# Kernel tuning notes

Measured on AMD Instinct MI355X. Metric: run time of the kernel, lower is better.

Reference implementation:

```python
import jax, jax.numpy as jnp
import numpy as np

B, S, D = 16, 2048, 64
SCALE = 1.0 / np.sqrt(np.float32(D))  # forward divides by sqrt(embedding_dim=64)


def setup_inputs() -> dict:
    key = jax.random.key(0)
    ks = jax.random.split(key, 7)
    return {
        "x": jax.random.normal(ks[0], (B, S, D), dtype=jnp.float32),
        "Wq": jax.random.normal(ks[1], (D, D), dtype=jnp.float32) * 0.02,
        "bq": jax.random.normal(ks[2], (D,), dtype=jnp.float32) * 0.02,
        "Wk": jax.random.normal(ks[3], (D, D), dtype=jnp.float32) * 0.02,
        "bk": jax.random.normal(ks[4], (D,), dtype=jnp.float32) * 0.02,
        "Wv": jax.random.normal(ks[5], (D, D), dtype=jnp.float32) * 0.02,
        "bv": jax.random.normal(ks[6], (D,), dtype=jnp.float32) * 0.02,
    }


def reference(x, Wq, bq, Wk, bk, Wv, bv):
    # Linear projections (weights stored [in, out], math-equivalent to nn.Linear)
    q = jnp.einsum("bsd,de->bse", x, Wq) + bq
    k = jnp.einsum("bsd,de->bse", x, Wk) + bk
    v = jnp.einsum("bsd,de->bse", x, Wv) + bv
    # Unfused scores: [B, S, S]
    scores = jnp.einsum("bqd,bkd->bqk", q, k) * jnp.float32(SCALE)
    causal = jnp.tril(jnp.ones((S, S), dtype=bool))  # mask[:S,:S]
    scores = jnp.where(causal, scores, jnp.float32(-jnp.inf))
    attn = jax.nn.softmax(scores, axis=-1)
    # dropout is identity in eval mode (reference baseline)
    out = jnp.einsum("bqk,bkd->bqd", attn, v)
    return out
```

## Files before the change

kernel.cpp:

```cpp
#include <hip/hip_runtime.h>

#define NB 16
#define SS 2048
#define DD 64

typedef __attribute__((ext_vector_type(8))) short short8;
typedef __attribute__((ext_vector_type(4))) float f32x4;

#define SCL2E 0.18033688011112042f

__device__ __forceinline__ short f2bf(float f) {
  union { float f; unsigned u; } v; v.f = f;
  unsigned r = (v.u + 0x7fffu + ((v.u >> 16) & 1u)) >> 16;
  return (short)r;
}

__device__ __forceinline__ short8 load_a_frag_f32(const float* p) {
  float4 u = *(const float4*)p;
  float4 w = *(const float4*)(p + 4);
  short8 r;
  r[0] = f2bf(u.x); r[1] = f2bf(u.y); r[2] = f2bf(u.z); r[3] = f2bf(u.w);
  r[4] = f2bf(w.x); r[5] = f2bf(w.y); r[6] = f2bf(w.z); r[7] = f2bf(w.w);
  return r;
}

__global__ __launch_bounds__(256) void proj_kernel(
    const float* __restrict__ x,
    const float* __restrict__ Wq, const float* __restrict__ bq,
    const float* __restrict__ Wk, const float* __restrict__ bk,
    const float* __restrict__ Wv, const float* __restrict__ bv,
    ushort* __restrict__ qo, ushort* __restrict__ ko, ushort* __restrict__ vT)
{
  __shared__ __align__(16) ushort Wt[3][64][72];
  __shared__ __align__(16) ushort Vs[64][68];
  const int t = threadIdx.x;
  {
    const float* Ws[3] = {Wq, Wk, Wv};
    for (int m = 0; m < 3; ++m)
      for (int i = 0; i < 4; ++i) {
        int idx = i * 1024 + t * 4;
        int kk = idx >> 6, n0 = idx & 63;
        float4 w4 = *(const float4*)(Ws[m] + kk * 64 + n0);
        Wt[m][n0 + 0][kk] = (ushort)f2bf(w4.x);
        Wt[m][n0 + 1][kk] = (ushort)f2bf(w4.y);
        Wt[m][n0 + 2][kk] = (ushort)f2bf(w4.z);
        Wt[m][n0 + 3][kk] = (ushort)f2bf(w4.w);
      }
  }
  __syncthreads();

  const int lane = t & 63, w = t >> 6;
  const int l15 = lane & 15, quad = lane >> 4;
  const int g = blockIdx.x * 64 + w * 16 + l15;
  short8 a0 = load_a_frag_f32(x + (size_t)g * 64 + quad * 8);
  short8 a1 = load_a_frag_f32(x + (size_t)g * 64 + 32 + quad * 8);
  const int lrow0 = w * 16 + quad * 4;
  const int row0 = blockIdx.x * 64 + lrow0;

  for (int m = 0; m < 3; ++m) {
    const float* bp = (m == 0 ? bq : (m == 1 ? bk : bv));
    for (int nt = 0; nt < 4; ++nt) {
      short8 b0 = *(const short8*)&Wt[m][nt * 16 + l15][quad * 8];
      short8 b1 = *(const short8*)&Wt[m][nt * 16 + l15][32 + quad * 8];
      f32x4 acc = {0.f, 0.f, 0.f, 0.f};
      acc = __builtin_amdgcn_mfma_f32_16x16x32_bf16(a0, b0, acc, 0, 0, 0);
      acc = __builtin_amdgcn_mfma_f32_16x16x32_bf16(a1, b1, acc, 0, 0, 0);
      float bb = bp[nt * 16 + l15];
      if (m == 0) {
        for (int r = 0; r < 4; ++r)
          qo[(size_t)(row0 + r) * 64 + nt * 16 + l15] = (ushort)f2bf(acc[r] + bb);
      } else if (m == 1) {
        for (int r = 0; r < 4; ++r)
          ko[(size_t)(row0 + r) * 64 + nt * 16 + l15] = (ushort)f2bf(acc[r] + bb);
      } else {
        for (int r = 0; r < 4; ++r)
          Vs[lrow0 + r][nt * 16 + l15] = (ushort)f2bf(acc[r] + bb);
      }
    }
  }
  __syncthreads();
  {
    const int batch = blockIdx.x >> 5;
    const int s0 = (blockIdx.x & 31) * 64;
    const int d = t >> 2, j0 = (t & 3) * 16;
    ushort tmp[16];
    for (int j = 0; j < 16; ++j) tmp[j] = Vs[j0 + j][d];
    ushort* dst = vT + (size_t)batch * DD * SS + (size_t)d * SS + s0 + j0;
    ((int4*)dst)[0] = ((int4*)tmp)[0];
    ((int4*)dst)[1] = ((int4*)tmp)[1];
  }
}

template<bool MASKED>
__device__ __forceinline__ void attn_half(
    const f32x4 (&c)[4], float (&l_part)[4], f32x4 (&acc)[4],
    const short8 (&vf0)[4], const short8 (&vf1)[4],
    ushort* __restrict__ Pw, int keyb, int rowb, int l15, int quad)
{
#pragma unroll
  for (int ct = 0; ct < 4; ++ct)
#pragma unroll
    for (int r = 0; r < 4; ++r) {
      float pe = __builtin_amdgcn_exp2f(c[ct][r] * SCL2E);
      if (MASKED && (keyb + ct * 16 > rowb + r)) pe = 0.f;
      l_part[r] += pe;
      Pw[(quad * 4 + r) * 72 + ct * 16 + l15] = (ushort)f2bf(pe);
    }
  short8 pa0 = *(const short8*)&Pw[l15 * 72 + quad * 8];
  short8 pa1 = *(const short8*)&Pw[l15 * 72 + 32 + quad * 8];
#pragma unroll
  for (int nt = 0; nt < 4; ++nt) {
    acc[nt] = __builtin_amdgcn_mfma_f32_16x16x32_bf16(pa0, vf0[nt], acc[nt], 0, 0, 0);
    acc[nt] = __builtin_amdgcn_mfma_f32_16x16x32_bf16(pa1, vf1[nt], acc[nt], 0, 0, 0);
  }
}

__global__ __launch_bounds__(256, 3) void attn_kernel(
    const ushort* __restrict__ qg, const ushort* __restrict__ kg,
    const ushort* __restrict__ vT, float* __restrict__ out)
{
  __shared__ __align__(16) float accW[4][32][68];
  __shared__ float lW[4][32];
  ushort* Pw_base = (ushort*)&accW[0][0][0];

  const int t = threadIdx.x, bid = blockIdx.x;
  const int batch = (bid & 7) * 2 + ((bid >> 3) & 1);
  const int qt = 63 - (bid >> 4);
  const int q0 = qt * 32;
  const int lane = t & 63, w = t >> 6;
  const int l15 = lane & 15, quad = lane >> 4;
  const size_t bbase = (size_t)batch * SS * DD;
  ushort* Pw = Pw_base + w * (16 * 72);

  const ushort* qp = qg + bbase + (size_t)(q0 + l15) * 64 + quad * 8;
  short8 a0 = *(const short8*)qp;
  short8 a1 = *(const short8*)(qp + 32);
  short8 a2 = *(const short8*)(qp + 16 * 64);
  short8 a3 = *(const short8*)(qp + 16 * 64 + 32);

  f32x4 acc0[4], acc1[4];
  float l0[4] = {0.f, 0.f, 0.f, 0.f}, l1[4] = {0.f, 0.f, 0.f, 0.f};
#pragma unroll
  for (int nt = 0; nt < 4; ++nt) {
    acc0[nt] = (f32x4){0.f, 0.f, 0.f, 0.f};
    acc1[nt] = (f32x4){0.f, 0.f, 0.f, 0.f};
  }

  const int ktotal = ((q0 + 31) >> 6) + 1;
  const ushort* kp0 = kg + bbase + (size_t)(w * 64 + l15) * 64 + quad * 8;
  const ushort* kp1 = kp0 + 2048;
  const ushort* vp0 = vT + bbase + (size_t)(l15) * SS + w * 64 + quad * 8;
  const ushort* vp1 = vp0 + 16 * SS;
  const ushort* vp2 = vp0 + 32 * SS;
  const ushort* vp3 = vp0 + 48 * SS;

  for (int kt = w; kt < ktotal; kt += 4) {
    short8 kf0[4], kf1[4], vf0[4], vf1[4];
    kf0[0] = *(const short8*)(kp0);
    kf1[0] = *(const short8*)(kp0 + 32);
    kf0[1] = *(const short8*)(kp0 + 1024);
    kf1[1] = *(const short8*)(kp0 + 1056);
    kf0[2] = *(const short8*)(kp1);
    kf1[2] = *(const short8*)(kp1 + 32);
    kf0[3] = *(const short8*)(kp1 + 1024);
    kf1[3] = *(const short8*)(kp1 + 1056);
    vf0[0] = *(const short8*)(vp0); vf1[0] = *(const short8*)(vp0 + 32);
    vf0[1] = *(const short8*)(vp1); vf1[1] = *(const short8*)(vp1 + 32);
    vf0[2] = *(const short8*)(vp2); vf1[2] = *(const short8*)(vp2 + 32);
    vf0[3] = *(const short8*)(vp3); vf1[3] = *(const short8*)(vp3 + 32);

    f32x4 c0[4], c1[4];
#pragma unroll
    for (int ct = 0; ct < 4; ++ct) {
      c0[ct] = (f32x4){0.f, 0.f, 0.f, 0.f};
      c0[ct] = __builtin_amdgcn_mfma_f32_16x16x32_bf16(a0, kf0[ct], c0[ct], 0, 0, 0);
      c0[ct] = __builtin_amdgcn_mfma_f32_16x16x32_bf16(a1, kf1[ct], c0[ct], 0, 0, 0);
      c1[ct] = (f32x4){0.f, 0.f, 0.f, 0.f};
      c1[ct] = __builtin_amdgcn_mfma_f32_16x16x32_bf16(a2, kf0[ct], c1[ct], 0, 0, 0);
      c1[ct] = __builtin_amdgcn_mfma_f32_16x16x32_bf16(a3, kf1[ct], c1[ct], 0, 0, 0);
    }

    const int kb = kt * 64;
    if (kt == ktotal - 1) {
      attn_half<true >(c0, l0, acc0, vf0, vf1, Pw, kb + l15, q0 + quad * 4, l15, quad);
      attn_half<true >(c1, l1, acc1, vf0, vf1, Pw, kb + l15, q0 + 16 + quad * 4, l15, quad);
    } else {
      attn_half<false>(c0, l0, acc0, vf0, vf1, Pw, kb + l15, q0 + quad * 4, l15, quad);
      attn_half<false>(c1, l1, acc1, vf0, vf1, Pw, kb + l15, q0 + 16 + quad * 4, l15, quad);
    }
    kp0 += 16384; kp1 += 16384;
    vp0 += 256; vp1 += 256; vp2 += 256; vp3 += 256;
  }

#pragma unroll
  for (int r = 0; r < 4; ++r)
    for (int off = 1; off < 16; off <<= 1) {
      l0[r] += __shfl_xor(l0[r], off, 64);
      l1[r] += __shfl_xor(l1[r], off, 64);
    }

  __syncthreads();
#pragma unroll
  for (int r = 0; r < 4; ++r)
#pragma unroll
    for (int nt = 0; nt < 4; ++nt) {
      accW[w][quad * 4 + r][nt * 16 + l15] = acc0[nt][r];
      accW[w][16 + quad * 4 + r][nt * 16 + l15] = acc1[nt][r];
    }
  if (l15 == 0)
#pragma unroll
    for (int r = 0; r < 4; ++r) {
      lW[w][quad * 4 + r] = l0[r];
      lW[w][16 + quad * 4 + r] = l1[r];
    }
  __syncthreads();

  {
    const int row = t >> 3, col0 = (t & 7) * 8;
    float den = lW[0][row] + lW[1][row] + lW[2][row] + lW[3][row];
    float iv = 1.0f / den;
    float4 oa = {0.f, 0.f, 0.f, 0.f}, ob = {0.f, 0.f, 0.f, 0.f};
#pragma unroll
    for (int ww = 0; ww < 4; ++ww) {
      float4 x0 = *(const float4*)&accW[ww][row][col0];
      float4 x1 = *(const float4*)&accW[ww][row][col0 + 4];
      oa.x += x0.x; oa.y += x0.y; oa.z += x0.z; oa.w += x0.w;
      ob.x += x1.x; ob.y += x1.y; ob.z += x1.z; ob.w += x1.w;
    }
    oa.x *= iv; oa.y *= iv; oa.z *= iv; oa.w *= iv;
    ob.x *= iv; ob.y *= iv; ob.z *= iv; ob.w *= iv;
    float* op = out + bbase + (size_t)(q0 + row) * 64 + col0;
    *(float4*)op = oa;
    *(float4*)(op + 4) = ob;
  }
}

extern "C" void kernel_launch(void* const* d_in, const int* in_sizes, int n_in,
                              void* d_out, int out_size, void* d_ws, size_t ws_size,
                              hipStream_t stream) {
  (void)in_sizes; (void)n_in; (void)out_size; (void)ws_size;
  const float* x  = (const float*)d_in[0];
  const float* Wq = (const float*)d_in[1];
  const float* bq = (const float*)d_in[2];
  const float* Wk = (const float*)d_in[3];
  const float* bk = (const float*)d_in[4];
  const float* Wv = (const float*)d_in[5];
  const float* bv = (const float*)d_in[6];
  float* out = (float*)d_out;

  ushort* qws = (ushort*)d_ws;
  ushort* kws = qws + (size_t)NB * SS * DD;
  ushort* vws = kws + (size_t)NB * SS * DD;

  proj_kernel<<<dim3(NB * SS / 64), dim3(256), 0, stream>>>(
      x, Wq, bq, Wk, bk, Wv, bv, qws, kws, vws);
  attn_kernel<<<dim3(NB * (SS / 32)), dim3(256), 0, stream>>>(
      qws, kws, vws, out);
}
```

Baseline: 116.8 us.

## Keep P in registers via transposed score MFMA and lane shuffles, prebuild bf16 weights

The score MFMA now takes its operands in swapped order, so each lane holds a row of S^T. The bf16 P fragments are then assembled with cross-lane shuffles and packed cvt instructions, with no round trip through LDS. The per-row sum reduction shrinks to two shuffles, and a syncthreads is dropped. Weight transposition and bf16 conversion move to a separate small kernel, which removes redundant per-block LDS weight prep in the projection. That kernel now writes packed, vectorized outputs, and s_setprio hints are added around the MFMA sections. The cost is one extra kernel launch and extra shuffle instructions.

```diff
diff --git a/kernel.cpp b/kernel.cpp
--- a/kernel.cpp
+++ b/kernel.cpp
@@ -13,6 +13,12 @@
   union { float f; unsigned u; } v; v.f = f;
   unsigned r = (v.u + 0x7fffu + ((v.u >> 16) & 1u)) >> 16;
   return (short)r;
+}
+
+__device__ __forceinline__ unsigned cvtpk_bf16(float lo, float hi) {
+  unsigned r;
+  asm("v_cvt_pk_bf16_f32 %0, %1, %2" : "=v"(r) : "v"(lo), "v"(hi));
+  return r;
 }
 
 __device__ __forceinline__ short8 load_a_frag_f32(const float* p) {
@@ -24,57 +30,64 @@
   return r;
 }
 
+__global__ __launch_bounds__(256) void wprep_kernel(
+    const float* __restrict__ Wq, const float* __restrict__ Wk,
+    const float* __restrict__ Wv, ushort* __restrict__ Wt)
+{
+  const float* Ws[3] = {Wq, Wk, Wv};
+  const int m = blockIdx.x;
+  const float* src = Ws[m];
+  ushort* dst = Wt + m * 4096;
+  const int t = threadIdx.x;
+#pragma unroll
+  for (int i = 0; i < 4; ++i) {
+    int idx = i * 1024 + t * 4;
+    int k = idx >> 6, n0 = idx & 63;
+    float4 w4 = *(const float4*)(src + idx);
+    dst[(n0 + 0) * 64 + k] = (ushort)f2bf(w4.x);
+    dst[(n0 + 1) * 64 + k] = (ushort)f2bf(w4.y);
+    dst[(n0 + 2) * 64 + k] = (ushort)f2bf(w4.z);
+    dst[(n0 + 3) * 64 + k] = (ushort)f2bf(w4.w);
+  }
+}
+
 __global__ __launch_bounds__(256) void proj_kernel(
-    const float* __restrict__ x,
-    const float* __restrict__ Wq, const float* __restrict__ bq,
-    const float* __restrict__ Wk, const float* __restrict__ bk,
-    const float* __restrict__ Wv, const float* __restrict__ bv,
+    const float* __restrict__ x, const ushort* __restrict__ Wt,
+    const float* __restrict__ bq, const float* __restrict__ bk,
+    const float* __restrict__ bv,
     ushort* __restrict__ qo, ushort* __restrict__ ko, ushort* __restrict__ vT)
 {
-  __shared__ __align__(16) ushort Wt[3][64][72];
   __shared__ __align__(16) ushort Vs[64][68];
   const int t = threadIdx.x;
-  {
-    const float* Ws[3] = {Wq, Wk, Wv};
-    for (int m = 0; m < 3; ++m)
-      for (int i = 0; i < 4; ++i) {
-        int idx = i * 1024 + t * 4;
-        int kk = idx >> 6, n0 = idx & 63;
-        float4 w4 = *(const float4*)(Ws[m] + kk * 64 + n0);
-        Wt[m][n0 + 0][kk] = (ushort)f2bf(w4.x);
-        Wt[m][n0 + 1][kk] = (ushort)f2bf(w4.y);
-        Wt[m][n0 + 2][kk] = (ushort)f2bf(w4.z);
-        Wt[m][n0 + 3][kk] = (ushort)f2bf(w4.w);
-      }
-  }
-  __syncthreads();
-
   const int lane = t & 63, w = t >> 6;
   const int l15 = lane & 15, quad = lane >> 4;
   const int g = blockIdx.x * 64 + w * 16 + l15;
-  short8 a0 = load_a_frag_f32(x + (size_t)g * 64 + quad * 8);
-  short8 a1 = load_a_frag_f32(x + (size_t)g * 64 + 32 + quad * 8);
-  const int lrow0 = w * 16 + quad * 4;
-  const int row0 = blockIdx.x * 64 + lrow0;
-
+  short8 b0 = load_a_frag_f32(x + (size_t)g * 64 + quad * 8);
+  short8 b1 = load_a_frag_f32(x + (size_t)g * 64 + 32 + quad * 8);
+  const int lrow = w * 16 + l15;
+
+#pragma unroll
   for (int m = 0; m < 3; ++m) {
     const float* bp = (m == 0 ? bq : (m == 1 ? bk : bv));
+    const ushort* wm = Wt + m * 4096;
+#pragma unroll
     for (int nt = 0; nt < 4; ++nt) {
-      short8 b0 = *(const short8*)&Wt[m][nt * 16 + l15][quad * 8];
-      short8 b1 = *(const short8*)&Wt[m][nt * 16 + l15][32 + quad * 8];
+      const ushort* ap = wm + (nt * 16 + l15) * 64 + quad * 8;
+      short8 a0 = *(const short8*)ap;
+      short8 a1 = *(const short8*)(ap + 32);
       f32x4 acc = {0.f, 0.f, 0.f, 0.f};
       acc = __builtin_amdgcn_mfma_f32_16x16x32_bf16(a0, b0, acc, 0, 0, 0);
       acc = __builtin_amdgcn_mfma_f32_16x16x32_bf16(a1, b1, acc, 0, 0, 0);
-      float bb = bp[nt * 16 + l15];
+      float4 bb = *(const float4*)(bp + nt * 16 + quad * 4);
+      unsigned p0 = cvtpk_bf16(acc[0] + bb.x, acc[1] + bb.y);
+      unsigned p1 = cvtpk_bf16(acc[2] + bb.z, acc[3] + bb.w);
+      uint2 pk; pk.x = p0; pk.y = p1;
       if (m == 0) {
-        for (int r = 0; r < 4; ++r)
-          qo[(size_t)(row0 + r) * 64 + nt * 16 + l15] = (ushort)f2bf(acc[r] + bb);
+        *(uint2*)(qo + (size_t)g * 64 + nt * 16 + quad * 4) = pk;
       } else if (m == 1) {
-        for (int r = 0; r < 4; ++r)
-          ko[(size_t)(row0 + r) * 64 + nt * 16 + l15] = (ushort)f2bf(acc[r] + bb);
+        *(uint2*)(ko + (size_t)g * 64 + nt * 16 + quad * 4) = pk;
       } else {
-        for (int r = 0; r < 4; ++r)
-          Vs[lrow0 + r][nt * 16 + l15] = (ushort)f2bf(acc[r] + bb);
+        *(uint2*)&Vs[lrow][nt * 16 + quad * 4] = pk;
       }
     }
   }
@@ -84,6 +97,7 @@
     const int s0 = (blockIdx.x & 31) * 64;
     const int d = t >> 2, j0 = (t & 3) * 16;
     ushort tmp[16];
+#pragma unroll
     for (int j = 0; j < 16; ++j) tmp[j] = Vs[j0 + j][d];
     ushort* dst = vT + (size_t)batch * DD * SS + (size_t)d * SS + s0 + j0;
     ((int4*)dst)[0] = ((int4*)tmp)[0];
@@ -91,28 +105,59 @@
   }
 }
 
+__device__ __forceinline__ short8 build_pa(unsigned A0, unsigned A1,
+                                           unsigned B0, unsigned B1, int quad) {
+  int xA0 = __shfl_xor((int)A0, 32);
+  int xA1 = __shfl_xor((int)A1, 32);
+  int xB0 = __shfl_xor((int)B0, 32);
+  int xB1 = __shfl_xor((int)B1, 32);
+  const bool hi = quad >= 2;
+  const bool odd = quad & 1;
+  int Lo0 = hi ? xB0 : (int)A0;
+  int Lo1 = hi ? xB1 : (int)A1;
+  int Hi0 = hi ? (int)B0 : xA0;
+  int Hi1 = hi ? (int)B1 : xA1;
+  int xLo0 = __shfl_xor(Lo0, 16);
+  int xLo1 = __shfl_xor(Lo1, 16);
+  int xHi0 = __shfl_xor(Hi0, 16);
+  int xHi1 = __shfl_xor(Hi1, 16);
+  int4 wv;
+  wv.x = odd ? xHi0 : Lo0;
+  wv.y = odd ? xHi1 : Lo1;
+  wv.z = odd ? Hi0 : xLo0;
+  wv.w = odd ? Hi1 : xLo1;
+  return *(short8*)&wv;
+}
+
 template<bool MASKED>
 __device__ __forceinline__ void attn_half(
-    const f32x4 (&c)[4], float (&l_part)[4], f32x4 (&acc)[4],
+    const f32x4 (&c)[4], float& l_acc, f32x4 (&acc)[4],
     const short8 (&vf0)[4], const short8 (&vf1)[4],
-    ushort* __restrict__ Pw, int keyb, int rowb, int l15, int quad)
+    int keybase, int qabs, int quad)
 {
-#pragma unroll
-  for (int ct = 0; ct < 4; ++ct)
+  unsigned pk[4][2];
+#pragma unroll
+  for (int ct = 0; ct < 4; ++ct) {
+    float pe[4];
 #pragma unroll
     for (int r = 0; r < 4; ++r) {
-      float pe = __builtin_amdgcn_exp2f(c[ct][r] * SCL2E);
-      if (MASKED && (keyb + ct * 16 > rowb + r)) pe = 0.f;
-      l_part[r] += pe;
-      Pw[(quad * 4 + r) * 72 + ct * 16 + l15] = (ushort)f2bf(pe);
-    }
-  short8 pa0 = *(const short8*)&Pw[l15 * 72 + quad * 8];
-  short8 pa1 = *(const short8*)&Pw[l15 * 72 + 32 + quad * 8];
+      float p = __builtin_amdgcn_exp2f(c[ct][r] * SCL2E);
+      if (MASKED && (keybase + ct * 16 + quad * 4 + r > qabs)) p = 0.f;
+      pe[r] = p;
+      l_acc += p;
+    }
+    pk[ct][0] = cvtpk_bf16(pe[0], pe[1]);
+    pk[ct][1] = cvtpk_bf16(pe[2], pe[3]);
+  }
+  short8 pa0 = build_pa(pk[0][0], pk[0][1], pk[1][0], pk[1][1], quad);
+  short8 pa1 = build_pa(pk[2][0], pk[2][1], pk[3][0], pk[3][1], quad);
+  __builtin_amdgcn_s_setprio(1);
 #pragma unroll
   for (int nt = 0; nt < 4; ++nt) {
     acc[nt] = __builtin_amdgcn_mfma_f32_16x16x32_bf16(pa0, vf0[nt], acc[nt], 0, 0, 0);
     acc[nt] = __builtin_amdgcn_mfma_f32_16x16x32_bf16(pa1, vf1[nt], acc[nt], 0, 0, 0);
   }
+  __builtin_amdgcn_s_setprio(0);
 }
 
 __global__ __launch_bounds__(256, 3) void attn_kernel(
@@ -121,7 +166,6 @@
 {
   __shared__ __align__(16) float accW[4][32][68];
   __shared__ float lW[4][32];
-  ushort* Pw_base = (ushort*)&accW[0][0][0];
 
   const int t = threadIdx.x, bid = blockIdx.x;
   const int batch = (bid & 7) * 2 + ((bid >> 3) & 1);
@@ -130,7 +174,6 @@
   const int lane = t & 63, w = t >> 6;
   const int l15 = lane & 15, quad = lane >> 4;
   const size_t bbase = (size_t)batch * SS * DD;
-  ushort* Pw = Pw_base + w * (16 * 72);
 
   const ushort* qp = qg + bbase + (size_t)(q0 + l15) * 64 + quad * 8;
   short8 a0 = *(const short8*)qp;
@@ -139,7 +182,7 @@
   short8 a3 = *(const short8*)(qp + 16 * 64 + 32);
 
   f32x4 acc0[4], acc1[4];
-  float l0[4] = {0.f, 0.f, 0.f, 0.f}, l1[4] = {0.f, 0.f, 0.f, 0.f};
+  float l0 = 0.f, l1 = 0.f;
 #pragma unroll
   for (int nt = 0; nt < 4; ++nt) {
     acc0[nt] = (f32x4){0.f, 0.f, 0.f, 0.f};
@@ -153,6 +196,8 @@
   const ushort* vp1 = vp0 + 16 * SS;
   const ushort* vp2 = vp0 + 32 * SS;
   const ushort* vp3 = vp0 + 48 * SS;
+
+  const int qabs0 = q0 + l15, qabs1 = q0 + 16 + l15;
 
   for (int kt = w; kt < ktotal; kt += 4) {
     short8 kf0[4], kf1[4], vf0[4], vf1[4];
@@ -170,36 +215,32 @@
     vf0[3] = *(const short8*)(vp3); vf1[3] = *(const short8*)(vp3 + 32);
 
     f32x4 c0[4], c1[4];
+    __builtin_amdgcn_s_setprio(1);
 #pragma unroll
     for (int ct = 0; ct < 4; ++ct) {
-      c0[ct] = (f32x4){0.f, 0.f, 0.f, 0.f};
-      c0[ct] = __builtin_amdgcn_mfma_f32_16x16x32_bf16(a0, kf0[ct], c0[ct], 0, 0, 0);
-      c0[ct] = __builtin_amdgcn_mfma_f32_16x16x32_bf16(a1, kf1[ct], c0[ct], 0, 0, 0);
-      c1[ct] = (f32x4){0.f, 0.f, 0.f, 0.f};
-      c1[ct] = __builtin_amdgcn_mfma_f32_16x16x32_bf16(a2, kf0[ct], c1[ct], 0, 0, 0);
-      c1[ct] = __builtin_amdgcn_mfma_f32_16x16x32_bf16(a3, kf1[ct], c1[ct], 0, 0, 0);
-    }
+      f32x4 z = {0.f, 0.f, 0.f, 0.f};
+      c0[ct] = __builtin_amdgcn_mfma_f32_16x16x32_bf16(kf0[ct], a0, z, 0, 0, 0);
+      c0[ct] = __builtin_amdgcn_mfma_f32_16x16x32_bf16(kf1[ct], a1, c0[ct], 0, 0, 0);
+      c1[ct] = __builtin_amdgcn_mfma_f32_16x16x32_bf16(kf0[ct], a2, z, 0, 0, 0);
+      c1[ct] = __builtin_amdgcn_mfma_f32_16x16x32_bf16(kf1[ct], a3, c1[ct], 0, 0, 0);
+    }
+    __builtin_amdgcn_s_setprio(0);
 
     const int kb = kt * 64;
     if (kt == ktotal - 1) {
-      attn_half<true >(c0, l0, acc0, vf0, vf1, Pw, kb + l15, q0 + quad * 4, l15, quad);
-      attn_half<true >(c1, l1, acc1, vf0, vf1, Pw, kb + l15, q0 + 16 + quad * 4, l15, quad);
+      attn_half<true >(c0, l0, acc0, vf0, vf1, kb, qabs0, quad);
+      attn_half<true >(c1, l1, acc1, vf0, vf1, kb, qabs1, quad);
     } else {
-      attn_half<false>(c0, l0, acc0, vf0, vf1, Pw, kb + l15, q0 + quad * 4, l15, quad);
-      attn_half<false>(c1, l1, acc1, vf0, vf1, Pw, kb + l15, q0 + 16 + quad * 4, l15, quad);
+      attn_half<false>(c0, l0, acc0, vf0, vf1, kb, qabs0, quad);
+      attn_half<false>(c1, l1, acc1, vf0, vf1, kb, qabs1, quad);
     }
     kp0 += 16384; kp1 += 16384;
     vp0 += 256; vp1 += 256; vp2 += 256; vp3 += 256;
   }
 
-#pragma unroll
-  for (int r = 0; r < 4; ++r)
-    for (int off = 1; off < 16; off <<= 1) {
-      l0[r] += __shfl_xor(l0[r], off, 64);
-      l1[r] += __shfl_xor(l1[r], off, 64);
-    }
-
-  __syncthreads();
+  l0 += __shfl_xor(l0, 16); l0 += __shfl_xor(l0, 32);
+  l1 += __shfl_xor(l1, 16); l1 += __shfl_xor(l1, 32);
+
 #pragma unroll
   for (int r = 0; r < 4; ++r)
 #pragma unroll
@@ -207,12 +248,10 @@
       accW[w][quad * 4 + r][nt * 16 + l15] = acc0[nt][r];
       accW[w][16 + quad * 4 + r][nt * 16 + l15] = acc1[nt][r];
     }
-  if (l15 == 0)
-#pragma unroll
-    for (int r = 0; r < 4; ++r) {
-      lW[w][quad * 4 + r] = l0[r];
-      lW[w][16 + quad * 4 + r] = l1[r];
-    }
+  if (lane < 16) {
+    lW[w][lane] = l0;
+    lW[w][16 + lane] = l1;
+  }
   __syncthreads();
 
   {
@@ -251,9 +290,11 @@
   ushort* qws = (ushort*)d_ws;
   ushort* kws = qws + (size_t)NB * SS * DD;
   ushort* vws = kws + (size_t)NB * SS * DD;
-
+  ushort* wt  = vws + (size_t)NB * SS * DD;
+
+  wprep_kernel<<<dim3(3), dim3(256), 0, stream>>>(Wq, Wk, Wv, wt);
   proj_kernel<<<dim3(NB * SS / 64), dim3(256), 0, stream>>>(
-      x, Wq, bq, Wk, bk, Wv, bv, qws, kws, vws);
+      x, wt, bq, bk, bv, qws, kws, vws);
   attn_kernel<<<dim3(NB * (SS / 32)), dim3(256), 0, stream>>>(
       qws, kws, vws, out);
 }
```

Measured after the change: 122.7 us. 1.05x slower.
